# Performance work log

Hardware: AMD Instinct MI355X
Metric: run time of the kernel (lower is better)

The kernel has to match this reference:

```python
import jax, jax.numpy as jnp
import numpy as np

PATCH = 14  # dinov2 patch size
LN_EPS = 1e-5


def setup_inputs() -> dict:
    key = jax.random.key(0)
    ks = jax.random.split(key, 6)
    Nb, P, E, Hd = 4096, 5476, 1024, 128  # boxes, patches (74*74), embed_dim, hidden_dim
    return {
        "patch_tokens": jax.random.normal(ks[0], (1, P, E), dtype=jnp.float32),
        "bboxes": jax.random.randint(ks[1], (Nb, 4), 0, 1036, dtype=jnp.int32),
        "H": 1036,
        "W": 1036,
        "W1": jax.random.normal(ks[2], (E, Hd), dtype=jnp.float32) * 0.02,
        "b1": jnp.zeros((Hd,), dtype=jnp.float32),
        "gamma": jnp.ones((Hd,), dtype=jnp.float32),
        "beta": jnp.zeros((Hd,), dtype=jnp.float32),
        "W2": jax.random.normal(ks[3], (Hd, Hd), dtype=jnp.float32) * 0.02,
        "b2": jnp.zeros((Hd,), dtype=jnp.float32),
    }


def _roi_pool(patch_tokens, bboxes, H, W):
    """Vectorized equivalent of VisionEncoder.roi_pool_patches.

    patch_tokens: (1, nph*npw, E); bboxes: (Nb, 4) int pixel coords.
    Returns (Nb, E) mean of patch tokens inside each box.
    """
    nph, npw = H // PATCH, W // PATCH
    Nb = bboxes.shape[0]
    x1, y1, x2, y2 = (bboxes[:, 0], bboxes[:, 1], bboxes[:, 2], bboxes[:, 3])
    f32 = jnp.float32
    # int() truncation in torch == astype(int32) for non-negative values
    px1 = (x1.astype(f32) / W * npw).astype(jnp.int32)
    px2 = (x2.astype(f32) / W * npw).astype(jnp.int32)
    py1 = (y1.astype(f32) / H * nph).astype(jnp.int32)
    py2 = (y2.astype(f32) / H * nph).astype(jnp.int32)
    px1 = jnp.clip(px1, 0, npw - 1)
    px2 = jnp.maximum(px1 + 1, jnp.minimum(px2, npw))
    py1 = jnp.clip(py1, 0, nph - 1)
    py2 = jnp.maximum(py1 + 1, jnp.minimum(py2, nph))
    # Box membership masks over the patch grid (ragged gather expressed densely)
    ay = jnp.arange(nph, dtype=jnp.int32)
    ax = jnp.arange(npw, dtype=jnp.int32)
    my = (ay[None, :] >= py1[:, None]) & (ay[None, :] < py2[:, None])  # (Nb, nph)
    mx = (ax[None, :] >= px1[:, None]) & (ax[None, :] < px2[:, None])  # (Nb, npw)
    mask = (my[:, :, None] & mx[:, None, :]).reshape(Nb, nph * npw)
    mask = mask.astype(patch_tokens.dtype)
    counts = mask.sum(axis=-1, keepdims=True)  # always >= 1 by construction
    pooled = (mask @ patch_tokens[0]) / counts  # (Nb, E)
    return pooled


def _projection(x, W1, b1, gamma, beta, W2, b2):
    h = x @ W1 + b1
    mu = h.mean(axis=-1, keepdims=True)
    var = ((h - mu) ** 2).mean(axis=-1, keepdims=True)
    h = (h - mu) * jax.lax.rsqrt(var + LN_EPS) * gamma + beta
    h = jax.nn.relu(h)
    return h @ W2 + b2


def reference(patch_tokens, bboxes, H, W, W1, b1, gamma, beta, W2, b2):
    pooled = _roi_pool(patch_tokens, bboxes, H, W)
    return _projection(pooled, W1, b1, gamma, beta, W2, b2)
```

## Files before the change

kernel.cpp:

```cpp
#include <hip/hip_runtime.h>


#define HD   128
#define SPLITK 8

typedef __attribute__((ext_vector_type(8))) short bf16x8;
typedef __attribute__((ext_vector_type(4))) float f32x4;

__device__ __forceinline__ int decode_dim(const int* p, int fallback) {
    if (p == nullptr) return fallback;
    int vi = *p;
    if (vi >= 1 && vi <= 1000000) return vi;
    float vf = __int_as_float(vi);
    if (vf >= 1.0f && vf <= 1000000.0f) return (int)vf;
    return fallback;
}

__attribute__((noinline, optnone))
__device__ int coord_map(int x, int W, int n) {
    double rd = 1.0 / (double)W;
    float r = (float)rd;
    double qd = (double)x * (double)r;
    float q = (float)qd;
    double pd = (double)q * (double)n;
    float p = (float)pd;
    return (int)p;
}

__device__ __forceinline__ unsigned short bf16_rne(float x) {
    unsigned u = __float_as_uint(x);
    unsigned r = u + 0x7fffu + ((u >> 16) & 1u);
    return (unsigned short)(r >> 16);
}

__global__ __launch_bounds__(256) void split_w1_kernel(
    const float* __restrict__ W1, unsigned short* __restrict__ Whi,
    unsigned short* __restrict__ Wlo, int E)
{
    __shared__ float tile[64][65];
    int t = threadIdx.x;
    int k0 = blockIdx.x * 64, n0 = blockIdx.y * 64;

    int r = t >> 4, c4 = (t & 15) * 4;
#pragma unroll
    for (int i = 0; i < 4; ++i) {
        int kr = r + i * 16;
        *(float4*)&tile[kr][c4] =
            *(const float4*)&W1[(size_t)(k0 + kr) * HD + n0 + c4];
    }
    __syncthreads();

    int nl = t >> 2, kq = (t & 3) * 16;
    unsigned hp[8], lp[8];
#pragma unroll
    for (int j = 0; j < 8; ++j) {
        float x0 = tile[kq + 2 * j][nl];
        float x1 = tile[kq + 2 * j + 1][nl];
        unsigned h0 = bf16_rne(x0);
        unsigned h1 = bf16_rne(x1);
        float l0 = x0 - __uint_as_float(h0 << 16);
        float l1 = x1 - __uint_as_float(h1 << 16);
        hp[j] = h0 | ((unsigned)h1 << 16);
        lp[j] = (unsigned)bf16_rne(l0) | ((unsigned)bf16_rne(l1) << 16);
    }
    size_t off = (size_t)(n0 + nl) * E + k0 + kq;
    *(uint4*)(Whi + off)     = make_uint4(hp[0], hp[1], hp[2], hp[3]);
    *(uint4*)(Whi + off + 8) = make_uint4(hp[4], hp[5], hp[6], hp[7]);
    *(uint4*)(Wlo + off)     = make_uint4(lp[0], lp[1], lp[2], lp[3]);
    *(uint4*)(Wlo + off + 8) = make_uint4(lp[4], lp[5], lp[6], lp[7]);
}

__global__ __launch_bounds__(256) void gemm_u_mfma(
    const float* __restrict__ T, const unsigned short* __restrict__ Whi,
    const unsigned short* __restrict__ Wlo, float* __restrict__ U,
    int P, int E)
{
    int t = threadIdx.x;
    int lane = t & 63;
    int w = t >> 6;
    int row0 = blockIdx.x * 32 + (w & 1) * 16;
    int col0 = (w >> 1) * 64;
    int kchunk = E >> 3;
    int kbase = blockIdx.y * kchunk;
    float* Uo = U + (size_t)blockIdx.y * (size_t)HD * P;

    int lr  = lane & 15;
    int lkq = (lane >> 4) * 8;

    int arow = row0 + lr; if (arow >= P) arow = P - 1;
    const float* ap = T + (size_t)arow * E + kbase + lkq;
    const unsigned short* bh0 = Whi + (size_t)(col0 + lr) * E + kbase + lkq;
    const unsigned short* bl0 = Wlo + (size_t)(col0 + lr) * E + kbase + lkq;

    float4 a[8];
#pragma unroll
    for (int s = 0; s < 4; ++s) {
        a[2 * s]     = *(const float4*)(ap + s * 32);
        a[2 * s + 1] = *(const float4*)(ap + s * 32 + 4);
    }

    f32x4 acc[4];
#pragma unroll
    for (int n = 0; n < 4; ++n) acc[n] = (f32x4){0.f, 0.f, 0.f, 0.f};

    bf16x8 bh[2][4], bl[2][4];
#pragma unroll
    for (int n = 0; n < 4; ++n) {
        bh[0][n] = *(const bf16x8*)(bh0 + (size_t)(n * 16) * E);
        bl[0][n] = *(const bf16x8*)(bl0 + (size_t)(n * 16) * E);
    }

#pragma unroll
    for (int s = 0; s < 4; ++s) {
        int cur = s & 1, nxt = cur ^ 1;
        if (s < 3) {
#pragma unroll
            for (int n = 0; n < 4; ++n) {
                bh[nxt][n] = *(const bf16x8*)(bh0 + (size_t)(n * 16) * E + (s + 1) * 32);
                bl[nxt][n] = *(const bf16x8*)(bl0 + (size_t)(n * 16) * E + (s + 1) * 32);
            }
        }
        float av[8] = {a[2 * s].x, a[2 * s].y, a[2 * s].z, a[2 * s].w,
                       a[2 * s + 1].x, a[2 * s + 1].y, a[2 * s + 1].z, a[2 * s + 1].w};
        bf16x8 ahi, alo;
#pragma unroll
        for (int j = 0; j < 8; ++j) {
            unsigned h = bf16_rne(av[j]);
            ahi[j] = (short)h;
            float l = av[j] - __uint_as_float(h << 16);
            alo[j] = (short)bf16_rne(l);
        }
#pragma unroll
        for (int n = 0; n < 4; ++n) {
            acc[n] = __builtin_amdgcn_mfma_f32_16x16x32_bf16(ahi, bh[cur][n], acc[n], 0, 0, 0);
            acc[n] = __builtin_amdgcn_mfma_f32_16x16x32_bf16(alo, bh[cur][n], acc[n], 0, 0, 0);
            acc[n] = __builtin_amdgcn_mfma_f32_16x16x32_bf16(ahi, bl[cur][n], acc[n], 0, 0, 0);
        }
    }

    int cr0 = row0 + (lane >> 4) * 4;
    int cc  = lane & 15;
    if (cr0 < P) {
#pragma unroll
        for (int n = 0; n < 4; ++n) {
            float4 v = make_float4(acc[n][0], acc[n][1], acc[n][2], acc[n][3]);
            *(float4*)&Uo[(size_t)(col0 + n * 16 + cc) * P + cr0] = v;
        }
    }
}

__global__ __launch_bounds__(512) void sat_kernel(
    const float* __restrict__ U, float* __restrict__ S,
    int P, int npw, int nph)
{
    extern __shared__ float tile[];
    int t = threadIdx.x;
    int c = blockIdx.x;
    int ldt = npw + 3;
    int PP = nph * npw;

    const float* Uc = U + (size_t)c * P;
    size_t ustride = (size_t)HD * P;

    for (int i = t; i < PP; i += 512) {
        float s = Uc[i];
#pragma unroll
        for (int p = 1; p < SPLITK; ++p) s += Uc[(size_t)p * ustride + i];
        int y = i / npw, x = i - y * npw;
        tile[(y + 1) * ldt + (x + 1)] = s;
    }
    if (t <= npw) tile[t] = 0.f;
    if (t <= nph) tile[t * ldt] = 0.f;
    __syncthreads();

    if (t < nph) {
        int row = (t + 1) * ldt;
        float a = 0.f;
        for (int x = 1; x <= npw; ++x) { a += tile[row + x]; tile[row + x] = a; }
    }
    __syncthreads();

    if (t < npw) {
        int col = t + 1;
        float a = 0.f;
        for (int y = 1; y <= nph; ++y) {
            a += tile[y * ldt + col]; tile[y * ldt + col] = a;
        }
    }
    __syncthreads();

    int tot = (nph + 1) * (npw + 1);
    for (int i = t; i < tot; i += 512) {
        int y = i / (npw + 1), x = i - y * (npw + 1);
        S[((size_t)y * (npw + 1) + x) * HD + c] = tile[y * ldt + x];
    }
}

__global__ __launch_bounds__(256) void pool_proj_kernel(
    const float* __restrict__ S, const int* __restrict__ bboxes,
    const int* __restrict__ pH, const int* __restrict__ pW,
    const float* __restrict__ b1, const float* __restrict__ gamma,
    const float* __restrict__ beta, const float* __restrict__ W2,
    const float* __restrict__ b2, float* __restrict__ out,
    int Nb, int npw, int nph, int fbW, int fbH)
{
    __shared__ float hs[16][HD + 1];
    __shared__ float Bs[32][HD];
    __shared__ float red_s[16][17], red_q[16][17];
    __shared__ int   cI11[16], cI12[16], cI21[16], cI22[16];
    __shared__ float cCnt[16];
    __shared__ float mu_s[16], rs_s[16];

    int t = threadIdx.x;
    int c = t & 127;
    int rh = t >> 7;
    int row0 = blockIdx.x * 16;

    if (t < 16) {
        int b = row0 + t; if (b >= Nb) b = Nb - 1;
        int x1 = bboxes[b * 4 + 0];
        int y1 = bboxes[b * 4 + 1];
        int x2 = bboxes[b * 4 + 2];
        int y2 = bboxes[b * 4 + 3];
        int Wi = decode_dim(pW, fbW);
        int Hi = decode_dim(pH, fbH);
        int px1 = coord_map(x1, Wi, npw);
        int px2 = coord_map(x2, Wi, npw);
        int py1 = coord_map(y1, Hi, nph);
        int py2 = coord_map(y2, Hi, nph);
        px1 = min(max(px1, 0), npw - 1);
        px2 = max(px1 + 1, min(px2, npw));
        py1 = min(max(py1, 0), nph - 1);
        py2 = max(py1 + 1, min(py2, nph));
        int st = npw + 1;
        cI11[t] = (py1 * st + px1) * HD;
        cI12[t] = (py1 * st + px2) * HD;
        cI21[t] = (py2 * st + px1) * HD;
        cI22[t] = (py2 * st + px2) * HD;
        cCnt[t] = (float)((py2 - py1) * (px2 - px1));
    }
    __syncthreads();

    float bias1 = b1[c];
    float hv[8];
#pragma unroll
    for (int r = 0; r < 8; ++r) {
        int row = rh * 8 + r;
        float s = S[cI22[row] + c] - S[cI12[row] + c]
                - S[cI21[row] + c] + S[cI11[row] + c];
        hv[r] = s / cCnt[row] + bias1;
        hs[row][c] = hv[r];
    }
    __syncthreads();

    {
        int sr = t & 15;
        int sg = t >> 4;
        float ps = 0.f, pq = 0.f;
#pragma unroll
        for (int i = 0; i < 8; ++i) {
            float v = hs[sr][sg * 8 + i];
            ps += v; pq += v * v;
        }
        red_s[sr][sg] = ps; red_q[sr][sg] = pq;
    }
    __syncthreads();
    if (t < 16) {
        float s = 0.f, q = 0.f;
#pragma unroll
        for (int i = 0; i < 16; ++i) { s += red_s[t][i]; q += red_q[t][i]; }
        float m = s * (1.0f / HD);
        float v = q * (1.0f / HD) - m * m;
        mu_s[t] = m;
        rs_s[t] = rsqrtf(v + 1e-5f);
    }
    __syncthreads();

    float g = gamma[c], be = beta[c];
#pragma unroll
    for (int r = 0; r < 8; ++r) {
        int row = rh * 8 + r;
        float x = (hv[r] - mu_s[row]) * rs_s[row] * g + be;
        hs[row][c] = fmaxf(x, 0.f);
    }
    __syncthreads();

    float bias2 = b2[c];
    float acc2[8];
#pragma unroll
    for (int r = 0; r < 8; ++r) acc2[r] = bias2;
    for (int k0 = 0; k0 < HD; k0 += 32) {
#pragma unroll
        for (int i = 0; i < 16; ++i) {
            int idx = t + i * 256;
            int kk = idx >> 7, cc = idx & 127;
            Bs[kk][cc] = W2[(size_t)(k0 + kk) * HD + cc];
        }
        __syncthreads();
#pragma unroll
        for (int kk = 0; kk < 32; ++kk) {
            float bv = Bs[kk][c];
#pragma unroll
            for (int r = 0; r < 8; ++r)
                acc2[r] += hs[rh * 8 + r][k0 + kk] * bv;
        }
        __syncthreads();
    }

#pragma unroll
    for (int r = 0; r < 8; ++r) {
        int rg = row0 + rh * 8 + r;
        if (rg < Nb) out[(size_t)rg * HD + c] = acc2[r];
    }
}

extern "C" void kernel_launch(void* const* d_in, const int* in_sizes, int n_in,
                              void* d_out, int out_size, void* d_ws, size_t ws_size,
                              hipStream_t stream) {
    int iT = 0, iB = 1, iH = 2, iW = 3, iW1 = 4, ib1 = 5, ig = 6, ibe = 7,
        iW2 = 8, ib2 = 9;
    bool has_scalars = (n_in >= 10 && in_sizes[2] == 1 && in_sizes[3] == 1);
    if (!has_scalars) { iW1 = 2; ib1 = 3; ig = 4; ibe = 5; iW2 = 6; ib2 = 7; }

    const float* tokens = (const float*)d_in[iT];
    const int*   bboxes = (const int*)d_in[iB];
    const int*   pH     = has_scalars ? (const int*)d_in[iH] : nullptr;
    const int*   pW     = has_scalars ? (const int*)d_in[iW] : nullptr;
    const float* W1     = (const float*)d_in[iW1];
    const float* b1     = (const float*)d_in[ib1];
    const float* gamma  = (const float*)d_in[ig];
    const float* beta   = (const float*)d_in[ibe];
    const float* W2     = (const float*)d_in[iW2];
    const float* b2     = (const float*)d_in[ib2];
    float* out = (float*)d_out;

    int Hd = in_sizes[ib1];
    int E  = in_sizes[iW1] / Hd;
    int Nb = in_sizes[iB] / 4;
    int P  = in_sizes[iT] / E;
    int npw = 1;
    while ((npw + 1) * (npw + 1) <= P) ++npw;
    int nph = P / npw;
    (void)out_size; (void)ws_size;

    float* S = (float*)d_ws;
    size_t s_elems = ((size_t)(nph + 1) * (npw + 1) * HD + 255) & ~(size_t)255;
    float* U = S + s_elems;
    size_t u_elems = ((size_t)SPLITK * HD * P + 255) & ~(size_t)255;
    unsigned short* Whi = (unsigned short*)(U + u_elems);
    unsigned short* Wlo = Whi + (size_t)E * HD;

    split_w1_kernel<<<dim3(E / 64, HD / 64), dim3(256), 0, stream>>>(
        W1, Whi, Wlo, E);

    int mtiles = (P + 31) / 32;
    gemm_u_mfma<<<dim3(mtiles, SPLITK), dim3(256), 0, stream>>>(
        tokens, Whi, Wlo, U, P, E);

    size_t sat_lds = (size_t)(nph + 1) * (npw + 3) * sizeof(float);
    sat_kernel<<<dim3(HD), dim3(512), sat_lds, stream>>>(
        U, S, P, npw, nph);

    pool_proj_kernel<<<dim3((Nb + 15) / 16), dim3(256), 0, stream>>>(
        S, bboxes, pH, pW, b1, gamma, beta, W2, b2, out, Nb, npw, nph,
        14 * npw, 14 * nph);
}
```

Measured before the change: 148.6 us.

## Drop split-K and W1 pre-split kernel; split W1 in-register inside full-K GEMM

Removes the separate kernel that converted W1 into transposed bf16 hi/lo arrays and the 8-way split-K partial buffers. The GEMM now loops over the full K range per block, loading fp32 W1 directly with strided scalar loads and splitting it into hi/lo inside registers. The SAT kernel no longer has to sum 8 partial planes. This saves a kernel launch and the partial-sum memory traffic, but each block now runs a serial loop over all of K. It also repeats the B-side conversion in every block and uses uncoalesced scalar loads of W1, with fewer total blocks.

```diff
diff --git a/kernel.cpp b/kernel.cpp
--- a/kernel.cpp
+++ b/kernel.cpp
@@ -1,8 +1,7 @@
 #include <hip/hip_runtime.h>
 
 
-#define HD   128
-#define SPLITK 8
+#define HD 128
 
 typedef __attribute__((ext_vector_type(8))) short bf16x8;
 typedef __attribute__((ext_vector_type(4))) float f32x4;
@@ -33,108 +32,76 @@
     return (unsigned short)(r >> 16);
 }
 
-__global__ __launch_bounds__(256) void split_w1_kernel(
-    const float* __restrict__ W1, unsigned short* __restrict__ Whi,
-    unsigned short* __restrict__ Wlo, int E)
-{
-    __shared__ float tile[64][65];
-    int t = threadIdx.x;
-    int k0 = blockIdx.x * 64, n0 = blockIdx.y * 64;
-
-    int r = t >> 4, c4 = (t & 15) * 4;
-#pragma unroll
-    for (int i = 0; i < 4; ++i) {
-        int kr = r + i * 16;
-        *(float4*)&tile[kr][c4] =
-            *(const float4*)&W1[(size_t)(k0 + kr) * HD + n0 + c4];
-    }
-    __syncthreads();
-
-    int nl = t >> 2, kq = (t & 3) * 16;
-    unsigned hp[8], lp[8];
-#pragma unroll
-    for (int j = 0; j < 8; ++j) {
-        float x0 = tile[kq + 2 * j][nl];
-        float x1 = tile[kq + 2 * j + 1][nl];
-        unsigned h0 = bf16_rne(x0);
-        unsigned h1 = bf16_rne(x1);
-        float l0 = x0 - __uint_as_float(h0 << 16);
-        float l1 = x1 - __uint_as_float(h1 << 16);
-        hp[j] = h0 | ((unsigned)h1 << 16);
-        lp[j] = (unsigned)bf16_rne(l0) | ((unsigned)bf16_rne(l1) << 16);
-    }
-    size_t off = (size_t)(n0 + nl) * E + k0 + kq;
-    *(uint4*)(Whi + off)     = make_uint4(hp[0], hp[1], hp[2], hp[3]);
-    *(uint4*)(Whi + off + 8) = make_uint4(hp[4], hp[5], hp[6], hp[7]);
-    *(uint4*)(Wlo + off)     = make_uint4(lp[0], lp[1], lp[2], lp[3]);
-    *(uint4*)(Wlo + off + 8) = make_uint4(lp[4], lp[5], lp[6], lp[7]);
-}
-
 __global__ __launch_bounds__(256) void gemm_u_mfma(
-    const float* __restrict__ T, const unsigned short* __restrict__ Whi,
-    const unsigned short* __restrict__ Wlo, float* __restrict__ U,
-    int P, int E)
+    const float* __restrict__ T, const float* __restrict__ W1,
+    float* __restrict__ U, int P, int E)
 {
     int t = threadIdx.x;
     int lane = t & 63;
     int w = t >> 6;
-    int row0 = blockIdx.x * 32 + (w & 1) * 16;
-    int col0 = (w >> 1) * 64;
-    int kchunk = E >> 3;
-    int kbase = blockIdx.y * kchunk;
-    float* Uo = U + (size_t)blockIdx.y * (size_t)HD * P;
-
+    int row0 = blockIdx.x * 16;
     int lr  = lane & 15;
     int lkq = (lane >> 4) * 8;
 
     int arow = row0 + lr; if (arow >= P) arow = P - 1;
-    const float* ap = T + (size_t)arow * E + kbase + lkq;
-    const unsigned short* bh0 = Whi + (size_t)(col0 + lr) * E + kbase + lkq;
-    const unsigned short* bl0 = Wlo + (size_t)(col0 + lr) * E + kbase + lkq;
-
-    float4 a[8];
-#pragma unroll
-    for (int s = 0; s < 4; ++s) {
-        a[2 * s]     = *(const float4*)(ap + s * 32);
-        a[2 * s + 1] = *(const float4*)(ap + s * 32 + 4);
-    }
-
-    f32x4 acc[4];
-#pragma unroll
-    for (int n = 0; n < 4; ++n) acc[n] = (f32x4){0.f, 0.f, 0.f, 0.f};
-
-    bf16x8 bh[2][4], bl[2][4];
-#pragma unroll
-    for (int n = 0; n < 4; ++n) {
-        bh[0][n] = *(const bf16x8*)(bh0 + (size_t)(n * 16) * E);
-        bl[0][n] = *(const bf16x8*)(bl0 + (size_t)(n * 16) * E);
-    }
-
-#pragma unroll
-    for (int s = 0; s < 4; ++s) {
-        int cur = s & 1, nxt = cur ^ 1;
-        if (s < 3) {
-#pragma unroll
-            for (int n = 0; n < 4; ++n) {
-                bh[nxt][n] = *(const bf16x8*)(bh0 + (size_t)(n * 16) * E + (s + 1) * 32);
-                bl[nxt][n] = *(const bf16x8*)(bl0 + (size_t)(n * 16) * E + (s + 1) * 32);
+    const float* ap = T + (size_t)arow * E + lkq;
+    const float* bp = W1 + (size_t)lkq * HD + w * 32 + lr;
+
+    f32x4 acc[2];
+    acc[0] = (f32x4){0.f, 0.f, 0.f, 0.f};
+    acc[1] = (f32x4){0.f, 0.f, 0.f, 0.f};
+
+    float ac[8], an[8], bc[2][8], bn[2][8];
+
+    {
+        float4 a0 = *(const float4*)(ap);
+        float4 a1 = *(const float4*)(ap + 4);
+        ac[0] = a0.x; ac[1] = a0.y; ac[2] = a0.z; ac[3] = a0.w;
+        ac[4] = a1.x; ac[5] = a1.y; ac[6] = a1.z; ac[7] = a1.w;
+#pragma unroll
+        for (int nn = 0; nn < 2; ++nn)
+#pragma unroll
+            for (int j = 0; j < 8; ++j)
+                bc[nn][j] = bp[(size_t)j * HD + nn * 16];
+    }
+
+    for (int kt = 0; kt < E; kt += 32) {
+        if (kt + 32 < E) {
+            float4 a0 = *(const float4*)(ap + kt + 32);
+            float4 a1 = *(const float4*)(ap + kt + 36);
+            an[0] = a0.x; an[1] = a0.y; an[2] = a0.z; an[3] = a0.w;
+            an[4] = a1.x; an[5] = a1.y; an[6] = a1.z; an[7] = a1.w;
+#pragma unroll
+            for (int nn = 0; nn < 2; ++nn)
+#pragma unroll
+                for (int j = 0; j < 8; ++j)
+                    bn[nn][j] = bp[(size_t)(kt + 32 + j) * HD + nn * 16];
+        }
+
+        bf16x8 ahi, alo;
+#pragma unroll
+        for (int j = 0; j < 8; ++j) {
+            unsigned h = bf16_rne(ac[j]);
+            ahi[j] = (short)h;
+            alo[j] = (short)bf16_rne(ac[j] - __uint_as_float(h << 16));
+        }
+#pragma unroll
+        for (int nn = 0; nn < 2; ++nn) {
+            bf16x8 bhi, blo;
+#pragma unroll
+            for (int j = 0; j < 8; ++j) {
+                unsigned h = bf16_rne(bc[nn][j]);
+                bhi[j] = (short)h;
+                blo[j] = (short)bf16_rne(bc[nn][j] - __uint_as_float(h << 16));
             }
-        }
-        float av[8] = {a[2 * s].x, a[2 * s].y, a[2 * s].z, a[2 * s].w,
-                       a[2 * s + 1].x, a[2 * s + 1].y, a[2 * s + 1].z, a[2 * s + 1].w};
-        bf16x8 ahi, alo;
+            acc[nn] = __builtin_amdgcn_mfma_f32_16x16x32_bf16(ahi, bhi, acc[nn], 0, 0, 0);
+            acc[nn] = __builtin_amdgcn_mfma_f32_16x16x32_bf16(alo, bhi, acc[nn], 0, 0, 0);
+            acc[nn] = __builtin_amdgcn_mfma_f32_16x16x32_bf16(ahi, blo, acc[nn], 0, 0, 0);
+        }
+
 #pragma unroll
         for (int j = 0; j < 8; ++j) {
-            unsigned h = bf16_rne(av[j]);
-            ahi[j] = (short)h;
-            float l = av[j] - __uint_as_float(h << 16);
-            alo[j] = (short)bf16_rne(l);
-        }
-#pragma unroll
-        for (int n = 0; n < 4; ++n) {
-            acc[n] = __builtin_amdgcn_mfma_f32_16x16x32_bf16(ahi, bh[cur][n], acc[n], 0, 0, 0);
-            acc[n] = __builtin_amdgcn_mfma_f32_16x16x32_bf16(alo, bh[cur][n], acc[n], 0, 0, 0);
-            acc[n] = __builtin_amdgcn_mfma_f32_16x16x32_bf16(ahi, bl[cur][n], acc[n], 0, 0, 0);
+            ac[j] = an[j]; bc[0][j] = bn[0][j]; bc[1][j] = bn[1][j];
         }
     }
 
@@ -142,9 +109,9 @@
     int cc  = lane & 15;
     if (cr0 < P) {
 #pragma unroll
-        for (int n = 0; n < 4; ++n) {
-            float4 v = make_float4(acc[n][0], acc[n][1], acc[n][2], acc[n][3]);
-            *(float4*)&Uo[(size_t)(col0 + n * 16 + cc) * P + cr0] = v;
+        for (int nn = 0; nn < 2; ++nn) {
+            float4 v = make_float4(acc[nn][0], acc[nn][1], acc[nn][2], acc[nn][3]);
+            *(float4*)&U[(size_t)(w * 32 + nn * 16 + cc) * P + cr0] = v;
         }
     }
 }
@@ -160,12 +127,9 @@
     int PP = nph * npw;
 
     const float* Uc = U + (size_t)c * P;
-    size_t ustride = (size_t)HD * P;
 
     for (int i = t; i < PP; i += 512) {
         float s = Uc[i];
-#pragma unroll
-        for (int p = 1; p < SPLITK; ++p) s += Uc[(size_t)p * ustride + i];
         int y = i / npw, x = i - y * npw;
         tile[(y + 1) * ldt + (x + 1)] = s;
     }
@@ -346,16 +310,10 @@
     float* S = (float*)d_ws;
     size_t s_elems = ((size_t)(nph + 1) * (npw + 1) * HD + 255) & ~(size_t)255;
     float* U = S + s_elems;
-    size_t u_elems = ((size_t)SPLITK * HD * P + 255) & ~(size_t)255;
-    unsigned short* Whi = (unsigned short*)(U + u_elems);
-    unsigned short* Wlo = Whi + (size_t)E * HD;
-
-    split_w1_kernel<<<dim3(E / 64, HD / 64), dim3(256), 0, stream>>>(
-        W1, Whi, Wlo, E);
-
-    int mtiles = (P + 31) / 32;
-    gemm_u_mfma<<<dim3(mtiles, SPLITK), dim3(256), 0, stream>>>(
-        tokens, Whi, Wlo, U, P, E);
+
+    int mtiles = (P + 15) / 16;
+    gemm_u_mfma<<<dim3(mtiles), dim3(256), 0, stream>>>(
+        tokens, W1, U, P, E);
 
     size_t sat_lds = (size_t)(nph + 1) * (npw + 3) * sizeof(float);
     sat_kernel<<<dim3(HD), dim3(512), sat_lds, stream>>>(
```

Result: faster. 145.4 us (-2.2%).
